# Kernel tuning notes

Measured on AMD Instinct MI355X. Metric: run time of the kernel, lower is better.

Reference implementation:

```python
import jax, jax.numpy as jnp
import numpy as np

B, S, H = 8, 512, 768
NH, DH = 12, 64
I = 3072
E = 8
TOPK = 2
EPS = 1e-12


def _ln(x, g, b):
    m = jnp.mean(x, axis=-1, keepdims=True)
    v = jnp.mean(jnp.square(x - m), axis=-1, keepdims=True)
    return (x - m) * jax.lax.rsqrt(v + EPS) * g + b


def setup_inputs() -> dict:
    key = jax.random.key(0)
    ks = jax.random.split(key, 20)
    s_h = 1.0 / np.sqrt(H)
    s_i = 1.0 / np.sqrt(I)
    inp = {
        "hidden_states": jax.random.normal(ks[0], (B, S, H), jnp.float32),
        "Wq": jax.random.normal(ks[1], (H, H), jnp.float32) * s_h,
        "bq": jnp.zeros((H,), jnp.float32),
        "Wk": jax.random.normal(ks[2], (H, H), jnp.float32) * s_h,
        "bk": jnp.zeros((H,), jnp.float32),
        "Wv": jax.random.normal(ks[3], (H, H), jnp.float32) * s_h,
        "bv": jnp.zeros((H,), jnp.float32),
        "Wo": jax.random.normal(ks[4], (H, H), jnp.float32) * s_h,
        "bo": jnp.zeros((H,), jnp.float32),
        "ln_attn_g": jnp.ones((H,), jnp.float32),
        "ln_attn_b": jnp.zeros((H,), jnp.float32),
        "ln_ffn_g": jnp.ones((H,), jnp.float32),
        "ln_ffn_b": jnp.zeros((H,), jnp.float32),
        "Wr": jax.random.normal(ks[5], (H, E), jnp.float32) * s_h,
        "br": jnp.zeros((E,), jnp.float32),
        "W_up": jax.random.normal(ks[6], (E, H, I), jnp.float32) * s_h,
        "b_up": jnp.zeros((E, I), jnp.float32),
        "W_new": jax.random.normal(ks[7], (E, H, I), jnp.float32) * s_h,
        "b_new": jnp.zeros((E, I), jnp.float32),
        "W_down": jax.random.normal(ks[8], (E, I, H), jnp.float32) * s_i,
        "b_down": jnp.zeros((E, H), jnp.float32),
    }
    return inp


def reference(hidden_states, Wq, bq, Wk, bk, Wv, bv, Wo, bo,
              ln_attn_g, ln_attn_b, ln_ffn_g, ln_ffn_b,
              Wr, br, W_up, b_up, W_new, b_new, W_down, b_down):
    x = hidden_states
    # --- BertSelfAttention ---
    q = (x @ Wq + bq).reshape(B, S, NH, DH).transpose(0, 2, 1, 3)
    k = (x @ Wk + bk).reshape(B, S, NH, DH).transpose(0, 2, 1, 3)
    v = (x @ Wv + bv).reshape(B, S, NH, DH).transpose(0, 2, 1, 3)
    scores = jnp.einsum("bhqd,bhkd->bhqk", q, k) / np.sqrt(DH)
    probs = jax.nn.softmax(scores, axis=-1)
    ctx = jnp.einsum("bhqk,bhkd->bhqd", probs, v)
    ctx = ctx.transpose(0, 2, 1, 3).reshape(B, S, H)
    # --- BertSelfOutput: dense + residual + LayerNorm ---
    attention_output = _ln(ctx @ Wo + bo + x, ln_attn_g, ln_attn_b)
    # --- feed_forward_chunk: LayerNorm then token top-k MoE ---
    xl = _ln(attention_output, ln_ffn_g, ln_ffn_b)
    router_logits = xl @ Wr + br                      # [B,S,E]
    router_probs = jax.nn.softmax(router_logits, axis=-1)
    topw, topi = jax.lax.top_k(router_probs, TOPK)    # [B,S,K]
    topw = topw / jnp.sum(topw, axis=-1, keepdims=True)
    gates = jnp.sum(jax.nn.one_hot(topi, E, dtype=xl.dtype) * topw[..., None], axis=-2)  # [B,S,E]
    # --- experts (BertExpert: gelu(up(x)) * new(x) -> down), dense over E ---
    up = jax.nn.gelu(jnp.einsum("bsh,ehi->ebsi", xl, W_up) + b_up[:, None, None, :], approximate=False)
    gate_h = jnp.einsum("bsh,ehi->ebsi", xl, W_new) + b_new[:, None, None, :]
    y = jnp.einsum("ebsi,eih->ebsh", up * gate_h, W_down) + b_down[:, None, None, :]
    moe_out = jnp.einsum("ebsh,bse->bsh", y, gates)
    layer_output = moe_out + attention_output
    return layer_output, router_logits
```

## Files before the change

kernel.cpp:

```cpp
#include <hip/hip_runtime.h>
#include <hip/hip_bf16.h>
#include <cmath>


constexpr int cB = 8, cS = 512, cH = 768, cNH = 12, cDH = 64, cI = 3072, cE = 8;
constexpr int cT = cB * cS;
constexpr size_t TH = (size_t)cT * cH;

typedef __hip_bfloat16 bf16;
typedef __attribute__((ext_vector_type(8))) short s8v;
typedef __attribute__((ext_vector_type(4))) float f4v;

constexpr size_t SZ_WEXP     = (size_t)cE * cI * cH / 2;
constexpr size_t OFF_WUP_T   = 0;
constexpr size_t OFF_WNEW_T  = OFF_WUP_T + SZ_WEXP;
constexpr size_t OFF_WDOWN_T = OFF_WNEW_T + SZ_WEXP;
constexpr size_t OFF_QKV     = OFF_WDOWN_T + SZ_WEXP;
constexpr size_t OFF_CTX     = OFF_QKV + 4 * TH;
constexpr size_t OFF_XLB     = OFF_CTX + TH;
constexpr size_t OFF_WGT     = OFF_XLB + TH / 2;
constexpr size_t OFF_COUNTS  = OFF_WGT + 2 * cT;
constexpr size_t OFF_LISTS   = OFF_COUNTS + 16;

__device__ __forceinline__ void glds16(const void* g, void* l) {
    __builtin_amdgcn_global_load_lds(
        (const __attribute__((address_space(1))) unsigned int*)g,
        (__attribute__((address_space(3))) unsigned int*)l, 16, 0, 0);
}

__global__ void init_counts_kernel(int* __restrict__ counts) {
    if (threadIdx.x < cE) counts[threadIdx.x] = 0;
}

__global__ __launch_bounds__(256) void transpose_bf16_kernel(
    const float* __restrict__ src, bf16* __restrict__ dst, int R, int C) {
    __shared__ float tile[64][65];
    const size_t zb = (size_t)blockIdx.z * R * C;
    const int r0 = blockIdx.y * 64, c0 = blockIdx.x * 64;
    const int t = threadIdx.x;
    const int lr = t >> 4, lc = (t & 15) * 4;
#pragma unroll
    for (int i = 0; i < 4; ++i) {
        float4 v = *(const float4*)(src + zb + (size_t)(r0 + lr + i * 16) * C + c0 + lc);
        tile[lr + i * 16][lc + 0] = v.x; tile[lr + i * 16][lc + 1] = v.y;
        tile[lr + i * 16][lc + 2] = v.z; tile[lr + i * 16][lc + 3] = v.w;
    }
    __syncthreads();
#pragma unroll
    for (int i = 0; i < 4; ++i) {
        int cr = lr + i * 16;
        bf16 o[4];
#pragma unroll
        for (int j = 0; j < 4; ++j) o[j] = (bf16)tile[lc + j][cr];
        *(uint2*)(dst + zb + (size_t)(c0 + cr) * R + r0 + lc) = *(uint2*)o;
    }
}

__device__ __forceinline__ void gemm_body64(
    const float* __restrict__ A, const float* __restrict__ B,
    const float* __restrict__ bias, float* __restrict__ C,
    int N, int K, int m0, int n0, int kbeg, int kend, bool addb) {
    __shared__ float As[16 * 68];
    __shared__ float Bs[16 * 128];
    const int t = threadIdx.x;
    const int tx = t & 15, ty = t >> 4;
    const int ar = t >> 2, ac = (t & 3) * 4;
    const float* gB0 = B + (size_t)kbeg * N + (size_t)(t >> 5) * N + n0 + (t & 31) * 4;
    float* dB0 = Bs + t * 4;
    float acc[4][8] = {};
    for (int k0 = kbeg; k0 < kend; k0 += 16) {
        float4 a0 = *(const float4*)(A + (size_t)(m0 + ar) * K + k0 + ac);
        glds16(gB0, dB0);
        glds16(gB0 + (size_t)8 * N, dB0 + 1024);
        As[(ac + 0) * 68 + ar] = a0.x; As[(ac + 1) * 68 + ar] = a0.y;
        As[(ac + 2) * 68 + ar] = a0.z; As[(ac + 3) * 68 + ar] = a0.w;
        __syncthreads();
#pragma unroll
        for (int kk = 0; kk < 16; ++kk) {
            float a[4], b[8];
            *(float4*)&a[0] = *(const float4*)&As[kk * 68 + ty * 4];
            *(float4*)&b[0] = *(const float4*)&Bs[kk * 128 + tx * 4];
            *(float4*)&b[4] = *(const float4*)&Bs[kk * 128 + tx * 4 + 64];
#pragma unroll
            for (int i = 0; i < 4; ++i)
#pragma unroll
                for (int j = 0; j < 8; ++j) acc[i][j] += a[i] * b[j];
        }
        __syncthreads();
        gB0 += (size_t)16 * N;
    }
#pragma unroll
    for (int i = 0; i < 4; ++i) {
        int m = m0 + ty * 4 + i;
        float4 o0, o1;
        o0.x = acc[i][0]; o0.y = acc[i][1]; o0.z = acc[i][2]; o0.w = acc[i][3];
        o1.x = acc[i][4]; o1.y = acc[i][5]; o1.z = acc[i][6]; o1.w = acc[i][7];
        if (addb) {
            o0.x += bias[n0 + tx * 4 + 0]; o0.y += bias[n0 + tx * 4 + 1];
            o0.z += bias[n0 + tx * 4 + 2]; o0.w += bias[n0 + tx * 4 + 3];
            o1.x += bias[n0 + 64 + tx * 4 + 0]; o1.y += bias[n0 + 64 + tx * 4 + 1];
            o1.z += bias[n0 + 64 + tx * 4 + 2]; o1.w += bias[n0 + 64 + tx * 4 + 3];
        }
        *(float4*)(C + (size_t)m * N + n0 + tx * 4) = o0;
        *(float4*)(C + (size_t)m * N + n0 + 64 + tx * 4) = o1;
    }
}

__global__ __launch_bounds__(256) void gemm_qkv_kernel(
    const float* __restrict__ A,
    const float* __restrict__ Wq, const float* __restrict__ Wk,
    const float* __restrict__ Wv,
    const float* __restrict__ bq, const float* __restrict__ bk,
    const float* __restrict__ bv,
    float* __restrict__ q, float* __restrict__ k, float* __restrict__ v) {
    const int z = blockIdx.z;
    const float* B = (z == 0) ? Wq : (z == 1) ? Wk : Wv;
    const float* bias = (z == 0) ? bq : (z == 1) ? bk : bv;
    float* C = (z == 0) ? q : (z == 1) ? k : v;
    gemm_body64(A, B, bias, C, cH, cH, blockIdx.y * 64, blockIdx.x * 128,
                0, cH, true);
}

__global__ __launch_bounds__(256) void gemm_wo_kernel(
    const float* __restrict__ A, const float* __restrict__ W,
    const float* __restrict__ bias,
    float* __restrict__ p0, float* __restrict__ p1) {
    const int ks = blockIdx.z;
    gemm_body64(A, W, bias, ks ? p1 : p0, cH, cH,
                blockIdx.y * 64, blockIdx.x * 128,
                ks * (cH / 2), ks * (cH / 2) + (cH / 2), ks == 0);
}

__global__ __launch_bounds__(256) void attn_kernel(
    const float* __restrict__ q, const float* __restrict__ k,
    const float* __restrict__ v, float* __restrict__ ctx) {
    __shared__ float sQ[64][68];
    __shared__ float sKV[64][68];
    __shared__ float sS[64][68];
    __shared__ float sM[64], sL[64], sAl[64];
    const int q0 = blockIdx.x * 64, h = blockIdx.y, b = blockIdx.z;
    const int t = threadIdx.x;
    const int lr = t >> 2, lq = (t & 3) * 16;
    {
        const float* gq = q + (size_t)(b * cS + q0 + lr) * cH + h * cDH + lq;
#pragma unroll
        for (int j = 0; j < 4; ++j) {
            float4 x = *(const float4*)(gq + j * 4);
            x.x *= 0.125f; x.y *= 0.125f; x.z *= 0.125f; x.w *= 0.125f;
            *(float4*)&sQ[lr][lq + j * 4] = x;
        }
    }
    if (t < 64) { sM[t] = -1e30f; sL[t] = 0.f; }
    const int c0 = t & 15, rr = (t >> 4) * 4;
    const int d4 = (t & 15) * 4, rp = (t >> 4) * 4;
    const int sr = t >> 2, sc = (t & 3) * 16;
    float4 o_acc[4];
#pragma unroll
    for (int i = 0; i < 4; ++i) o_acc[i] = make_float4(0.f, 0.f, 0.f, 0.f);

    for (int kt = 0; kt < 8; ++kt) {
        float4 kreg[4];
        {
            const float* gk = k + (size_t)(b * cS + kt * 64 + lr) * cH + h * cDH + lq;
#pragma unroll
            for (int j = 0; j < 4; ++j) kreg[j] = *(const float4*)(gk + j * 4);
        }
        __syncthreads();
#pragma unroll
        for (int j = 0; j < 4; ++j) *(float4*)&sKV[lr][lq + j * 4] = kreg[j];
        __syncthreads();
        float accS[4][4] = {};
#pragma unroll
        for (int d = 0; d < 64; d += 4) {
            float4 qv[4], kv[4];
#pragma unroll
            for (int i = 0; i < 4; ++i) qv[i] = *(const float4*)&sQ[rr + i][d];
#pragma unroll
            for (int j = 0; j < 4; ++j) kv[j] = *(const float4*)&sKV[c0 + 16 * j][d];
#pragma unroll
            for (int i = 0; i < 4; ++i)
#pragma unroll
                for (int j = 0; j < 4; ++j)
                    accS[i][j] += qv[i].x * kv[j].x + qv[i].y * kv[j].y +
                                  qv[i].z * kv[j].z + qv[i].w * kv[j].w;
        }
#pragma unroll
        for (int i = 0; i < 4; ++i)
#pragma unroll
            for (int j = 0; j < 4; ++j) sS[rr + i][c0 + 16 * j] = accS[i][j];
        float4 vreg[4];
        {
            const float* gv = v + (size_t)(b * cS + kt * 64 + lr) * cH + h * cDH + lq;
#pragma unroll
            for (int j = 0; j < 4; ++j) vreg[j] = *(const float4*)(gv + j * 4);
        }
        __syncthreads();
        {
            float4 s[4];
#pragma unroll
            for (int j = 0; j < 4; ++j) s[j] = *(const float4*)&sS[sr][sc + j * 4];
            float m = -1e30f;
#pragma unroll
            for (int j = 0; j < 4; ++j)
                m = fmaxf(m, fmaxf(fmaxf(s[j].x, s[j].y), fmaxf(s[j].z, s[j].w)));
            m = fmaxf(m, __shfl_xor(m, 1));
            m = fmaxf(m, __shfl_xor(m, 2));
            float m_old = sM[sr];
            float m_new = fmaxf(m_old, m);
            float sum = 0.f;
#pragma unroll
            for (int j = 0; j < 4; ++j) {
                s[j].x = __expf(s[j].x - m_new); s[j].y = __expf(s[j].y - m_new);
                s[j].z = __expf(s[j].z - m_new); s[j].w = __expf(s[j].w - m_new);
                sum += s[j].x + s[j].y + s[j].z + s[j].w;
                *(float4*)&sS[sr][sc + j * 4] = s[j];
            }
            sum += __shfl_xor(sum, 1);
            sum += __shfl_xor(sum, 2);
            if ((t & 3) == 0) {
                float alpha = __expf(m_old - m_new);
                sAl[sr] = alpha;
                sM[sr] = m_new;
                sL[sr] = sL[sr] * alpha + sum;
            }
        }
#pragma unroll
        for (int j = 0; j < 4; ++j) *(float4*)&sKV[lr][lq + j * 4] = vreg[j];
        __syncthreads();
#pragma unroll
        for (int i = 0; i < 4; ++i) {
            float al = sAl[rp + i];
            o_acc[i].x *= al; o_acc[i].y *= al; o_acc[i].z *= al; o_acc[i].w *= al;
        }
        for (int kk4 = 0; kk4 < 64; kk4 += 4) {
            float4 pv[4], vv[4];
#pragma unroll
            for (int i = 0; i < 4; ++i) pv[i] = *(const float4*)&sS[rp + i][kk4];
#pragma unroll
            for (int j = 0; j < 4; ++j) vv[j] = *(const float4*)&sKV[kk4 + j][d4];
#pragma unroll
            for (int i = 0; i < 4; ++i) {
                o_acc[i].x += pv[i].x * vv[0].x + pv[i].y * vv[1].x +
                              pv[i].z * vv[2].x + pv[i].w * vv[3].x;
                o_acc[i].y += pv[i].x * vv[0].y + pv[i].y * vv[1].y +
                              pv[i].z * vv[2].y + pv[i].w * vv[3].y;
                o_acc[i].z += pv[i].x * vv[0].z + pv[i].y * vv[1].z +
                              pv[i].z * vv[2].z + pv[i].w * vv[3].z;
                o_acc[i].w += pv[i].x * vv[0].w + pv[i].y * vv[1].w +
                              pv[i].z * vv[2].w + pv[i].w * vv[3].w;
            }
        }
    }
    __syncthreads();
#pragma unroll
    for (int i = 0; i < 4; ++i) {
        float inv = 1.0f / sL[rp + i];
        float4 o = o_acc[i];
        o.x *= inv; o.y *= inv; o.z *= inv; o.w *= inv;
        *(float4*)(ctx + (size_t)(b * cS + q0 + rp + i) * cH + h * cDH + d4) = o;
    }
}

__device__ __forceinline__ float block_reduce_sum(float v, float* red) {
#pragma unroll
    for (int o = 32; o; o >>= 1) v += __shfl_xor(v, o);
    __syncthreads();
    if ((threadIdx.x & 63) == 0) red[threadIdx.x >> 6] = v;
    __syncthreads();
    return red[0] + red[1] + red[2] + red[3];
}

__global__ __launch_bounds__(256) void ln_router_kernel(
    const float* __restrict__ dense0, const float* __restrict__ dense1,
    const float* __restrict__ resid,
    const float* __restrict__ g1, const float* __restrict__ b1,
    const float* __restrict__ g2, const float* __restrict__ b2,
    const float* __restrict__ Wr, const float* __restrict__ br,
    float* __restrict__ out, bf16* __restrict__ xlb,
    float* __restrict__ out_logits, float* __restrict__ wgt,
    int* __restrict__ counts, int* __restrict__ lists) {
    __shared__ float red[4];
    __shared__ float lred[4][8];
    const int t = blockIdx.x, tid = threadIdx.x;
    const size_t base = (size_t)t * cH;
    float v[3], s = 0.f;
#pragma unroll
    for (int i = 0; i < 3; ++i) {
        v[i] = dense0[base + tid + 256 * i] + dense1[base + tid + 256 * i] +
               resid[base + tid + 256 * i];
        s += v[i];
    }
    const float mean = block_reduce_sum(s, red) * (1.0f / cH);
    float vs = 0.f;
#pragma unroll
    for (int i = 0; i < 3; ++i) { float d = v[i] - mean; vs += d * d; }
    const float rstd = rsqrtf(block_reduce_sum(vs, red) * (1.0f / cH) + 1e-12f);
    float a[3], s2 = 0.f;
#pragma unroll
    for (int i = 0; i < 3; ++i) {
        a[i] = (v[i] - mean) * rstd * g1[tid + 256 * i] + b1[tid + 256 * i];
        out[base + tid + 256 * i] = a[i];
        s2 += a[i];
    }
    const float mean2 = block_reduce_sum(s2, red) * (1.0f / cH);
    float vs2 = 0.f;
#pragma unroll
    for (int i = 0; i < 3; ++i) { float d = a[i] - mean2; vs2 += d * d; }
    const float rstd2 = rsqrtf(block_reduce_sum(vs2, red) * (1.0f / cH) + 1e-12f);
    float xl[3];
#pragma unroll
    for (int i = 0; i < 3; ++i) {
        xl[i] = (a[i] - mean2) * rstd2 * g2[tid + 256 * i] + b2[tid + 256 * i];
        xlb[base + tid + 256 * i] = (bf16)xl[i];
    }
    float lg[cE] = {};
#pragma unroll
    for (int i = 0; i < 3; ++i) {
        const float* wr = Wr + (size_t)(tid + 256 * i) * cE;
#pragma unroll
        for (int e = 0; e < cE; ++e) lg[e] += xl[i] * wr[e];
    }
#pragma unroll
    for (int e = 0; e < cE; ++e)
#pragma unroll
        for (int o = 32; o; o >>= 1) lg[e] += __shfl_xor(lg[e], o);
    if ((tid & 63) == 0)
#pragma unroll
        for (int e = 0; e < cE; ++e) lred[tid >> 6][e] = lg[e];
    __syncthreads();
    if (tid == 0) {
        float logits[cE];
#pragma unroll
        for (int e = 0; e < cE; ++e) {
            logits[e] = lred[0][e] + lred[1][e] + lred[2][e] + lred[3][e] + br[e];
            out_logits[(size_t)t * cE + e] = logits[e];
        }
        int i0 = 0;
        for (int e = 1; e < cE; ++e) if (logits[e] > logits[i0]) i0 = e;
        int i1 = (i0 == 0) ? 1 : 0;
        for (int e = 0; e < cE; ++e)
            if (e != i0 && logits[e] > logits[i1]) i1 = e;
        float e1 = __expf(logits[i1] - logits[i0]);
        float w0 = 1.0f / (1.0f + e1);
        float w1 = e1 * w0;
        wgt[t * 2 + 0] = w0;
        wgt[t * 2 + 1] = w1;
        int p0 = atomicAdd(&counts[i0], 1);
        lists[i0 * cT + p0] = t * 2 + 0;
        int p1 = atomicAdd(&counts[i1], 1);
        lists[i1 * cT + p1] = t * 2 + 1;
    }
}

__global__ __launch_bounds__(256) void expert_up_mfma_kernel(
    const bf16* __restrict__ xlb,
    const bf16* __restrict__ WupT, const bf16* __restrict__ WnewT,
    const float* __restrict__ b_up, const float* __restrict__ b_new,
    const int* __restrict__ counts, const int* __restrict__ lists,
    bf16* __restrict__ act) {
    const int e = blockIdx.z;
    const int cnt = counts[e];
    const int m0 = blockIdx.y * 128;
    if (m0 >= cnt) return;
    const int n0 = blockIdx.x * 64;
    __shared__ short sA[128 * 32], sB1[64 * 32], sB2[64 * 32];
    __shared__ int rowa[128];
    const int t = threadIdx.x;
    if (t < 128) {
        int idx = m0 + t;
        rowa[t] = (idx < cnt) ? lists[e * cT + idx] : -1;
    }
    __syncthreads();
    const int lane = t & 63, w = t >> 6;
    const int wm = (w >> 1) * 64, wn = (w & 1) * 32;
    const int rA0 = t >> 2, kc8 = (t & 3) * 8;
    int a0 = rowa[rA0], a1 = rowa[rA0 + 64];
    const bf16* gA0 = xlb + (size_t)(a0 < 0 ? 0 : (a0 >> 1)) * cH + kc8;
    const bf16* gA1 = xlb + (size_t)(a1 < 0 ? 0 : (a1 >> 1)) * cH + kc8;
    const bf16* B1 = WupT + (size_t)e * cI * cH;
    const bf16* B2 = WnewT + (size_t)e * cI * cH;
    const bf16* gB1 = B1 + (size_t)(n0 + rA0) * cH + kc8;
    const bf16* gB2 = B2 + (size_t)(n0 + rA0) * cH + kc8;
    short* dA0 = sA + t * 8;   short* dA1 = sA + (t + 256) * 8;
    short* dB1 = sB1 + t * 8;  short* dB2 = sB2 + t * 8;
    f4v zero = {0.f, 0.f, 0.f, 0.f};
    f4v acc1[4][2], acc2[4][2];
#pragma unroll
    for (int i = 0; i < 4; ++i)
#pragma unroll
        for (int j = 0; j < 2; ++j) { acc1[i][j] = zero; acc2[i][j] = zero; }
    const int fr = lane & 15, kg = (lane >> 4) * 8;
    for (int kk = 0; kk < cH; kk += 32) {
        glds16(gA0, dA0); glds16(gA1, dA1);
        glds16(gB1, dB1); glds16(gB2, dB2);
        __syncthreads();
        s8v af[4], bf1[2], bf2[2];
#pragma unroll
        for (int i = 0; i < 4; ++i)
            af[i] = *(const s8v*)(sA + (wm + i * 16 + fr) * 32 + kg);
#pragma unroll
        for (int j = 0; j < 2; ++j) {
            bf1[j] = *(const s8v*)(sB1 + (wn + j * 16 + fr) * 32 + kg);
            bf2[j] = *(const s8v*)(sB2 + (wn + j * 16 + fr) * 32 + kg);
        }
#pragma unroll
        for (int mi = 0; mi < 4; ++mi)
#pragma unroll
            for (int ni = 0; ni < 2; ++ni) {
                acc1[mi][ni] = __builtin_amdgcn_mfma_f32_16x16x32_bf16(
                    af[mi], bf1[ni], acc1[mi][ni], 0, 0, 0);
                acc2[mi][ni] = __builtin_amdgcn_mfma_f32_16x16x32_bf16(
                    af[mi], bf2[ni], acc2[mi][ni], 0, 0, 0);
            }
        __syncthreads();
        gA0 += 32; gA1 += 32; gB1 += 32; gB2 += 32;
    }
    const int cn = lane & 15, rq = (lane >> 4) * 4;
#pragma unroll
    for (int mi = 0; mi < 4; ++mi)
#pragma unroll
        for (int r = 0; r < 4; ++r) {
            int ml = wm + mi * 16 + rq + r;
            int a = rowa[ml];
            if (a < 0) continue;
            bf16* orow = act + (size_t)a * cI + n0 + wn;
#pragma unroll
            for (int ni = 0; ni < 2; ++ni) {
                int nl = ni * 16 + cn;
                float up = acc1[mi][ni][r] + b_up[e * cI + n0 + wn + nl];
                float nw = acc2[mi][ni][r] + b_new[e * cI + n0 + wn + nl];
                float g = 0.5f * up * (1.0f + erff(up * 0.70710678118654752f));
                orow[nl] = (bf16)(g * nw);
            }
        }
}

__global__ __launch_bounds__(256) void expert_down_mfma_kernel(
    const bf16* __restrict__ act, const bf16* __restrict__ WdownT,
    const float* __restrict__ b_down,
    const int* __restrict__ counts, const int* __restrict__ lists,
    const float* __restrict__ wgt, float* __restrict__ out) {
    const int e = blockIdx.z;
    const int cnt = counts[e];
    const int m0 = blockIdx.y * 128;
    if (m0 >= cnt) return;
    const int n0 = blockIdx.x * 128;
    __shared__ short sA[128 * 32], sB[128 * 32];
    __shared__ int rowa[128];
    const int t = threadIdx.x;
    if (t < 128) {
        int idx = m0 + t;
        rowa[t] = (idx < cnt) ? lists[e * cT + idx] : -1;
    }
    __syncthreads();
    const int lane = t & 63, w = t >> 6;
    const int wm = (w >> 1) * 64, wn = (w & 1) * 64;
    const int rA0 = t >> 2, kc8 = (t & 3) * 8;
    int a0 = rowa[rA0], a1 = rowa[rA0 + 64];
    const bf16* gA0 = act + (size_t)(a0 < 0 ? 0 : a0) * cI + kc8;
    const bf16* gA1 = act + (size_t)(a1 < 0 ? 0 : a1) * cI + kc8;
    const bf16* BT = WdownT + (size_t)e * cH * cI;
    const bf16* gB0 = BT + (size_t)(n0 + rA0) * cI + kc8;
    const bf16* gB1 = BT + (size_t)(n0 + rA0 + 64) * cI + kc8;
    short* dA0 = sA + t * 8;       short* dA1 = sA + (t + 256) * 8;
    short* dB0 = sB + t * 8;       short* dB1 = sB + (t + 256) * 8;
    f4v zero = {0.f, 0.f, 0.f, 0.f};
    f4v acc[4][4];
#pragma unroll
    for (int i = 0; i < 4; ++i)
#pragma unroll
        for (int j = 0; j < 4; ++j) acc[i][j] = zero;
    const int fr = lane & 15, kg = (lane >> 4) * 8;
    for (int kk = 0; kk < cI; kk += 32) {
        glds16(gA0, dA0); glds16(gA1, dA1);
        glds16(gB0, dB0); glds16(gB1, dB1);
        __syncthreads();
        s8v af[4], bf[4];
#pragma unroll
        for (int i = 0; i < 4; ++i) af[i] = *(const s8v*)(sA + (wm + i * 16 + fr) * 32 + kg);
#pragma unroll
        for (int i = 0; i < 4; ++i) bf[i] = *(const s8v*)(sB + (wn + i * 16 + fr) * 32 + kg);
#pragma unroll
        for (int mi = 0; mi < 4; ++mi)
#pragma unroll
            for (int ni = 0; ni < 4; ++ni)
                acc[mi][ni] = __builtin_amdgcn_mfma_f32_16x16x32_bf16(
                    af[mi], bf[ni], acc[mi][ni], 0, 0, 0);
        __syncthreads();
        gA0 += 32; gA1 += 32; gB0 += 32; gB1 += 32;
    }
    const int cn = lane & 15, rq = (lane >> 4) * 4;
#pragma unroll
    for (int mi = 0; mi < 4; ++mi)
#pragma unroll
        for (int r = 0; r < 4; ++r) {
            int ml = wm + mi * 16 + rq + r;
            int a = rowa[ml];
            if (a < 0) continue;
            int token = a >> 1;
            float wv = wgt[a];
#pragma unroll
            for (int ni = 0; ni < 4; ++ni) {
                int n = n0 + wn + ni * 16 + cn;
                atomicAdd(&out[(size_t)token * cH + n],
                          wv * (acc[mi][ni][r] + b_down[e * cH + n]));
            }
        }
}

extern "C" void kernel_launch(void* const* d_in, const int* in_sizes, int n_in,
                              void* d_out, int out_size, void* d_ws, size_t ws_size,
                              hipStream_t stream) {
    const float* x      = (const float*)d_in[0];
    const float* Wq     = (const float*)d_in[1];
    const float* bq     = (const float*)d_in[2];
    const float* Wk     = (const float*)d_in[3];
    const float* bk     = (const float*)d_in[4];
    const float* Wv     = (const float*)d_in[5];
    const float* bv     = (const float*)d_in[6];
    const float* Wo     = (const float*)d_in[7];
    const float* bo     = (const float*)d_in[8];
    const float* ln1g   = (const float*)d_in[9];
    const float* ln1b   = (const float*)d_in[10];
    const float* ln2g   = (const float*)d_in[11];
    const float* ln2b   = (const float*)d_in[12];
    const float* Wr     = (const float*)d_in[13];
    const float* br     = (const float*)d_in[14];
    const float* W_up   = (const float*)d_in[15];
    const float* b_up   = (const float*)d_in[16];
    const float* W_new  = (const float*)d_in[17];
    const float* b_new  = (const float*)d_in[18];
    const float* W_down = (const float*)d_in[19];
    const float* b_down = (const float*)d_in[20];

    float* out = (float*)d_out;
    float* ws  = (float*)d_ws;

    bf16* WupT   = (bf16*)(ws + OFF_WUP_T);
    bf16* WnewT  = (bf16*)(ws + OFF_WNEW_T);
    bf16* WdownT = (bf16*)(ws + OFF_WDOWN_T);
    float* q     = ws + OFF_QKV;
    float* k     = ws + OFF_QKV + TH;
    float* v     = ws + OFF_QKV + 2 * TH;
    float* tmp   = ws + OFF_QKV + 3 * TH;
    bf16* act    = (bf16*)(ws + OFF_QKV);
    float* ctx   = ws + OFF_CTX;
    bf16* xlb    = (bf16*)(ws + OFF_XLB);
    float* wgt   = ws + OFF_WGT;
    int* counts  = (int*)(ws + OFF_COUNTS);
    int* lists   = (int*)(ws + OFF_LISTS);

    init_counts_kernel<<<1, 64, 0, stream>>>(counts);

    transpose_bf16_kernel<<<dim3(48, 12, cE), 256, 0, stream>>>(W_up, WupT, cH, cI);
    transpose_bf16_kernel<<<dim3(48, 12, cE), 256, 0, stream>>>(W_new, WnewT, cH, cI);
    transpose_bf16_kernel<<<dim3(12, 48, cE), 256, 0, stream>>>(W_down, WdownT, cI, cH);

    gemm_qkv_kernel<<<dim3(cH / 128, cT / 64, 3), 256, 0, stream>>>(
        x, Wq, Wk, Wv, bq, bk, bv, q, k, v);
    attn_kernel<<<dim3(cS / 64, cNH, cB), 256, 0, stream>>>(q, k, v, ctx);
    gemm_wo_kernel<<<dim3(cH / 128, cT / 64, 2), 256, 0, stream>>>(
        ctx, Wo, bo, q, k);
    ln_router_kernel<<<cT, 256, 0, stream>>>(
        q, k, x, ln1g, ln1b, ln2g, ln2b, Wr, br,
        out, xlb, out + TH, wgt, counts, lists);

    expert_up_mfma_kernel<<<dim3(cI / 64, cT / 128, cE), 256, 0, stream>>>(
        xlb, WupT, WnewT, b_up, b_new, counts, lists, act);
    expert_down_mfma_kernel<<<dim3(cH / 128, cT / 128, cE), 256, 0, stream>>>(
        act, WdownT, b_down, counts, lists, wgt, out);
}
```

Baseline: 1.052 ms.

## Enlarge fp32 GEMM tiles to 128x128 and add split-K for QKV and Wo

The shared SIMT GEMM body now computes 128x128 output tiles, so each thread holds an 8x8 accumulator, which raises reuse of each loaded A and B element. To keep enough blocks in flight, the QKV projection is split over K into two halves. Each half writes its partial sums to spare workspace buffers, and a new reduce kernel adds the halves together. The Wo projection is split four ways, and the LayerNorm/router kernel now sums four partial buffers plus the residual. The cost is one extra kernel launch, extra global memory traffic for the partial sums, and higher register pressure per thread.

```diff
diff --git a/kernel.cpp b/kernel.cpp
--- a/kernel.cpp
+++ b/kernel.cpp
@@ -56,33 +56,37 @@
     }
 }
 
-__device__ __forceinline__ void gemm_body64(
+__device__ __forceinline__ void gemm_body128(
     const float* __restrict__ A, const float* __restrict__ B,
     const float* __restrict__ bias, float* __restrict__ C,
     int N, int K, int m0, int n0, int kbeg, int kend, bool addb) {
-    __shared__ float As[16 * 68];
+    __shared__ float As[16 * 132];
     __shared__ float Bs[16 * 128];
     const int t = threadIdx.x;
     const int tx = t & 15, ty = t >> 4;
     const int ar = t >> 2, ac = (t & 3) * 4;
-    const float* gB0 = B + (size_t)kbeg * N + (size_t)(t >> 5) * N + n0 + (t & 31) * 4;
+    const float* gB0 = B + (size_t)(kbeg + (t >> 5)) * N + n0 + (t & 31) * 4;
     float* dB0 = Bs + t * 4;
-    float acc[4][8] = {};
+    float acc[8][8] = {};
     for (int k0 = kbeg; k0 < kend; k0 += 16) {
         float4 a0 = *(const float4*)(A + (size_t)(m0 + ar) * K + k0 + ac);
+        float4 a1 = *(const float4*)(A + (size_t)(m0 + ar + 64) * K + k0 + ac);
         glds16(gB0, dB0);
         glds16(gB0 + (size_t)8 * N, dB0 + 1024);
-        As[(ac + 0) * 68 + ar] = a0.x; As[(ac + 1) * 68 + ar] = a0.y;
-        As[(ac + 2) * 68 + ar] = a0.z; As[(ac + 3) * 68 + ar] = a0.w;
+        As[(ac + 0) * 132 + ar] = a0.x; As[(ac + 1) * 132 + ar] = a0.y;
+        As[(ac + 2) * 132 + ar] = a0.z; As[(ac + 3) * 132 + ar] = a0.w;
+        As[(ac + 0) * 132 + ar + 64] = a1.x; As[(ac + 1) * 132 + ar + 64] = a1.y;
+        As[(ac + 2) * 132 + ar + 64] = a1.z; As[(ac + 3) * 132 + ar + 64] = a1.w;
         __syncthreads();
 #pragma unroll
         for (int kk = 0; kk < 16; ++kk) {
-            float a[4], b[8];
-            *(float4*)&a[0] = *(const float4*)&As[kk * 68 + ty * 4];
+            float a[8], b[8];
+            *(float4*)&a[0] = *(const float4*)&As[kk * 132 + ty * 8];
+            *(float4*)&a[4] = *(const float4*)&As[kk * 132 + ty * 8 + 4];
             *(float4*)&b[0] = *(const float4*)&Bs[kk * 128 + tx * 4];
             *(float4*)&b[4] = *(const float4*)&Bs[kk * 128 + tx * 4 + 64];
 #pragma unroll
-            for (int i = 0; i < 4; ++i)
+            for (int i = 0; i < 8; ++i)
 #pragma unroll
                 for (int j = 0; j < 8; ++j) acc[i][j] += a[i] * b[j];
         }
@@ -90,8 +94,8 @@
         gB0 += (size_t)16 * N;
     }
 #pragma unroll
-    for (int i = 0; i < 4; ++i) {
-        int m = m0 + ty * 4 + i;
+    for (int i = 0; i < 8; ++i) {
+        int m = m0 + ty * 8 + i;
         float4 o0, o1;
         o0.x = acc[i][0]; o0.y = acc[i][1]; o0.z = acc[i][2]; o0.w = acc[i][3];
         o1.x = acc[i][4]; o1.y = acc[i][5]; o1.z = acc[i][6]; o1.w = acc[i][7];
@@ -112,23 +116,49 @@
     const float* __restrict__ Wv,
     const float* __restrict__ bq, const float* __restrict__ bk,
     const float* __restrict__ bv,
-    float* __restrict__ q, float* __restrict__ k, float* __restrict__ v) {
+    float* __restrict__ q0, float* __restrict__ k0, float* __restrict__ v0,
+    float* __restrict__ q1, float* __restrict__ k1, float* __restrict__ v1) {
     const int z = blockIdx.z;
-    const float* B = (z == 0) ? Wq : (z == 1) ? Wk : Wv;
-    const float* bias = (z == 0) ? bq : (z == 1) ? bk : bv;
-    float* C = (z == 0) ? q : (z == 1) ? k : v;
-    gemm_body64(A, B, bias, C, cH, cH, blockIdx.y * 64, blockIdx.x * 128,
-                0, cH, true);
+    const int p = z >> 1, ks = z & 1;
+    const float* B = (p == 0) ? Wq : (p == 1) ? Wk : Wv;
+    const float* bias = (p == 0) ? bq : (p == 1) ? bk : bv;
+    float* C = (p == 0) ? (ks ? q1 : q0)
+             : (p == 1) ? (ks ? k1 : k0)
+                        : (ks ? v1 : v0);
+    gemm_body128(A, B, bias, C, cH, cH, blockIdx.y * 128, blockIdx.x * 128,
+                 ks * 384, ks * 384 + 384, ks == 0);
+}
+
+__global__ __launch_bounds__(256) void reduce_qkv_kernel(
+    float* __restrict__ dst2, const float* __restrict__ src2,
+    float* __restrict__ v0, const float* __restrict__ v1) {
+    const size_t n2 = 2 * TH / 4, n3 = 3 * TH / 4;
+    for (size_t i = (size_t)blockIdx.x * 256 + threadIdx.x; i < n3;
+         i += (size_t)gridDim.x * 256) {
+        if (i < n2) {
+            float4 a = ((const float4*)dst2)[i];
+            float4 b = ((const float4*)src2)[i];
+            a.x += b.x; a.y += b.y; a.z += b.z; a.w += b.w;
+            ((float4*)dst2)[i] = a;
+        } else {
+            size_t j = i - n2;
+            float4 a = ((const float4*)v0)[j];
+            float4 b = ((const float4*)v1)[j];
+            a.x += b.x; a.y += b.y; a.z += b.z; a.w += b.w;
+            ((float4*)v0)[j] = a;
+        }
+    }
 }
 
 __global__ __launch_bounds__(256) void gemm_wo_kernel(
     const float* __restrict__ A, const float* __restrict__ W,
     const float* __restrict__ bias,
-    float* __restrict__ p0, float* __restrict__ p1) {
+    float* __restrict__ p0, float* __restrict__ p1,
+    float* __restrict__ p2, float* __restrict__ p3) {
     const int ks = blockIdx.z;
-    gemm_body64(A, W, bias, ks ? p1 : p0, cH, cH,
-                blockIdx.y * 64, blockIdx.x * 128,
-                ks * (cH / 2), ks * (cH / 2) + (cH / 2), ks == 0);
+    float* C = (ks == 0) ? p0 : (ks == 1) ? p1 : (ks == 2) ? p2 : p3;
+    gemm_body128(A, W, bias, C, cH, cH, blockIdx.y * 128, blockIdx.x * 128,
+                 ks * 192, ks * 192 + 192, ks == 0);
 }
 
 __global__ __launch_bounds__(256) void attn_kernel(
@@ -272,6 +302,7 @@
 
 __global__ __launch_bounds__(256) void ln_router_kernel(
     const float* __restrict__ dense0, const float* __restrict__ dense1,
+    const float* __restrict__ dense2, const float* __restrict__ dense3,
     const float* __restrict__ resid,
     const float* __restrict__ g1, const float* __restrict__ b1,
     const float* __restrict__ g2, const float* __restrict__ b2,
@@ -286,8 +317,8 @@
     float v[3], s = 0.f;
 #pragma unroll
     for (int i = 0; i < 3; ++i) {
-        v[i] = dense0[base + tid + 256 * i] + dense1[base + tid + 256 * i] +
-               resid[base + tid + 256 * i];
+        size_t ix = base + tid + 256 * i;
+        v[i] = dense0[ix] + dense1[ix] + dense2[ix] + dense3[ix] + resid[ix];
         s += v[i];
     }
     const float mean = block_reduce_sum(s, red) * (1.0f / cH);
@@ -556,13 +587,14 @@
     transpose_bf16_kernel<<<dim3(48, 12, cE), 256, 0, stream>>>(W_new, WnewT, cH, cI);
     transpose_bf16_kernel<<<dim3(12, 48, cE), 256, 0, stream>>>(W_down, WdownT, cI, cH);
 
-    gemm_qkv_kernel<<<dim3(cH / 128, cT / 64, 3), 256, 0, stream>>>(
-        x, Wq, Wk, Wv, bq, bk, bv, q, k, v);
+    gemm_qkv_kernel<<<dim3(cH / 128, cT / 128, 6), 256, 0, stream>>>(
+        x, Wq, Wk, Wv, bq, bk, bv, q, k, v, tmp, ctx, out);
+    reduce_qkv_kernel<<<2048, 256, 0, stream>>>(q, tmp, v, out);
     attn_kernel<<<dim3(cS / 64, cNH, cB), 256, 0, stream>>>(q, k, v, ctx);
-    gemm_wo_kernel<<<dim3(cH / 128, cT / 64, 2), 256, 0, stream>>>(
-        ctx, Wo, bo, q, k);
+    gemm_wo_kernel<<<dim3(cH / 128, cT / 128, 4), 256, 0, stream>>>(
+        ctx, Wo, bo, q, k, v, tmp);
     ln_router_kernel<<<cT, 256, 0, stream>>>(
-        q, k, x, ln1g, ln1b, ln2g, ln2b, Wr, br,
+        q, k, v, tmp, x, ln1g, ln1b, ln2g, ln2b, Wr, br,
         out, xlb, out + TH, wgt, counts, lists);
 
     expert_up_mfma_kernel<<<dim3(cI / 64, cT / 128, cE), 256, 0, stream>>>(
```

After: 1.051 ms. Within noise of the previous version (-0.1%).
